# Kernel tuning notes

Hardware: AMD Instinct MI355X
Metric: run time of the kernel (lower is better)

Reference implementation:

```python
import jax, jax.numpy as jnp
import numpy as np

NUM_HEADS = 8
NEG_INF = -1e9  # stand-in for -inf in the causal mask (avoids nan under masked softmax)


def setup_inputs() -> dict:
    key = jax.random.key(0)
    ks = jax.random.split(key, 8)
    B, C, H, W = 2, 512, 64, 64
    E = 512
    s = 1.0 / np.sqrt(C)
    return {
        "query": jax.random.normal(ks[0], (B, C, H, W), jnp.float32),
        "key": jax.random.normal(ks[1], (B, C, H, W), jnp.float32),
        "Wq": jax.random.normal(ks[2], (E, C), jnp.float32) * s,
        "bq": jax.random.normal(ks[3], (E,), jnp.float32) * 0.01,
        "Wk": jax.random.normal(ks[4], (E, C), jnp.float32) * s,
        "bk": jax.random.normal(ks[5], (E,), jnp.float32) * 0.01,
        "Wv": jax.random.normal(ks[6], (E, C), jnp.float32) * s,
        "bv": jax.random.normal(ks[7], (E,), jnp.float32) * 0.01,
    }


def reference(query, key, Wq, bq, Wk, bk, Wv, bv):
    B, qdim, H, W = query.shape
    N = H * W
    E = Wq.shape[0]
    nh = NUM_HEADS
    hd = E // nh

    # (B, C, H, W) -> (B, N, C)
    q_tok = query.transpose(0, 2, 3, 1).reshape(B, N, qdim)
    k_tok = key.transpose(0, 2, 3, 1).reshape(B, N, key.shape[1])

    q = (q_tok @ Wq.T + bq).reshape(B, N, nh, hd)
    k = (k_tok @ Wk.T + bk).reshape(B, N, nh, hd)
    v = (k_tok @ Wv.T + bv).reshape(B, N, nh, hd)

    # scores: (B, heads, N, N)
    scores = jnp.einsum("bqhd,bkhd->bhqk", q, k) / jnp.sqrt(jnp.float32(hd))
    causal = jnp.tril(jnp.ones((N, N), dtype=bool))
    scores = jnp.where(causal, scores, NEG_INF)
    attn = jax.nn.softmax(scores, axis=-1)  # dropout p=0.0 -> identity

    x = jnp.einsum("bhqk,bkhd->bhqd", attn, v)  # (B, h, N, hd)
    # permute to (B, h, hd, N) then view as (B, E, H, W) — matches torch ordering
    out = x.transpose(0, 1, 3, 2).reshape(B, E, H, W)
    return out
```

## Files before the change

kernel.cpp:

```cpp
#include <hip/hip_runtime.h>


typedef __bf16 bf16;
typedef __attribute__((ext_vector_type(8))) __bf16 bf16x8;
typedef __attribute__((ext_vector_type(4))) float floatx4;

#define B_ 2
#define Cc 512
#define Nn 4096
#define Ee 512
#define NH 8
#define HD 64

#define QSCALE 0.1803368801111204f

#define WSEG 262144
#define WTOT 787968

__device__ __forceinline__ int probe_f32(const unsigned short* w, int tid) {
  bool bad = false;
#pragma unroll
  for (int i = 0; i < 16; ++i) {
    unsigned u = w[(tid & 63) * 16 + i];
    float v = __uint_as_float(u << 16);
    bad |= !(v > -1024.f && v < 1024.f);
  }
  return (__ballot(bad) != 0ull) ? 1 : 0;
}

__device__ __forceinline__ bf16x8 load8e(const void* base, size_t eidx, int f32) {
  if (!f32) return *(const bf16x8*)((const bf16*)base + eidx);
  const float* f = (const float*)base + eidx;
  float4 a = *(const float4*)f;
  float4 c = *(const float4*)(f + 4);
  union { bf16 h[8]; bf16x8 v; } u;
  u.h[0] = (bf16)a.x; u.h[1] = (bf16)a.y; u.h[2] = (bf16)a.z; u.h[3] = (bf16)a.w;
  u.h[4] = (bf16)c.x; u.h[5] = (bf16)c.y; u.h[6] = (bf16)c.z; u.h[7] = (bf16)c.w;
  return u.v;
}

__global__ __launch_bounds__(256) void prep(
    const void* __restrict__ X0, const void* __restrict__ X1,
    bf16* __restrict__ T0, bf16* __restrict__ T1,
    const float* __restrict__ Wq, const float* __restrict__ Wk,
    const float* __restrict__ Wv, const float* __restrict__ bq,
    const float* __restrict__ bk, const float* __restrict__ bv,
    bf16* __restrict__ Wb) {
  const int f32 = probe_f32((const unsigned short*)Wq, (int)threadIdx.x);
  if (blockIdx.z == 4) {
    if (!f32) return;
    int task = (int)blockIdx.y * 64 + (int)blockIdx.x;
    int idx = (task * 256 + (int)threadIdx.x) * 8;
    if (idx >= WTOT) return;
    const float* src;
    int off;
    if (idx < WSEG)            { src = Wq; off = idx; }
    else if (idx < 2 * WSEG)   { src = Wk; off = idx - WSEG; }
    else if (idx < 3 * WSEG)   { src = Wv; off = idx - 2 * WSEG; }
    else if (idx < 3 * WSEG + 512)  { src = bq; off = idx - 3 * WSEG; }
    else if (idx < 3 * WSEG + 1024) { src = bk; off = idx - 3 * WSEG - 512; }
    else                            { src = bv; off = idx - 3 * WSEG - 1024; }
    float4 a = *(const float4*)(src + off);
    float4 c = *(const float4*)(src + off + 4);
    union { bf16 h[8]; bf16x8 v; } u;
    u.h[0] = (bf16)a.x; u.h[1] = (bf16)a.y; u.h[2] = (bf16)a.z; u.h[3] = (bf16)a.w;
    u.h[4] = (bf16)c.x; u.h[5] = (bf16)c.y; u.h[6] = (bf16)c.z; u.h[7] = (bf16)c.w;
    *(bf16x8*)(Wb + idx) = u.v;
    return;
  }
  __shared__ __align__(16) bf16 T[64 * 64];
  const int z = blockIdx.z;
  const int bb = z & 1;
  const void* src = (z >> 1) ? X1 : X0;
  bf16* dst = (z >> 1) ? T1 : T0;
  const int n0 = blockIdx.x * 64, c0 = blockIdx.y * 64;
  const int t = threadIdx.x;
  const size_t sbase = ((size_t)bb * Cc + c0) * (size_t)Nn + n0;

#pragma unroll
  for (int it = 0; it < 2; ++it) {
    int task = t + it * 256;
    int crow = task >> 3, gr = task & 7;
    bf16x8 v = load8e(src, sbase + (size_t)crow * Nn + gr * 8, f32);
    int slot = gr ^ (crow & 7);
    *(bf16x8*)&T[crow * 64 + slot * 8] = v;
  }
  __syncthreads();
  const int nrow = t & 63, cp = t >> 6;
  bf16* db = dst + ((size_t)bb * Nn + n0 + nrow) * Cc + c0;
#pragma unroll
  for (int it = 0; it < 2; ++it) {
    int cg = cp * 2 + it;
    union { bf16 h[8]; bf16x8 v; } u;
#pragma unroll
    for (int j = 0; j < 8; ++j) {
      int c = cg * 8 + j;
      int slot = (nrow >> 3) ^ (c & 7);
      u.h[j] = T[c * 64 + slot * 8 + (nrow & 7)];
    }
    *(bf16x8*)(db + cg * 8) = u.v;
  }
}

__global__ __launch_bounds__(256) void gemm3(
    const bf16* __restrict__ Xtq, const bf16* __restrict__ Xtk,
    const void* __restrict__ Wq0, const bf16* __restrict__ Wqb,
    const void* __restrict__ Wk0, const bf16* __restrict__ Wkb,
    const void* __restrict__ Wv0, const bf16* __restrict__ Wvb,
    const void* __restrict__ bq0, const bf16* __restrict__ bqb,
    const void* __restrict__ bk0, const bf16* __restrict__ bkb,
    const void* __restrict__ bv0, const bf16* __restrict__ bvb,
    bf16* __restrict__ Qt, bf16* __restrict__ Kt, bf16* __restrict__ Vh,
    int zoff) {
  const int f32 = probe_f32((const unsigned short*)Wq0, (int)threadIdx.x);
  const int z = (int)blockIdx.z + zoff;
  const int op = z >> 1, b = z & 1;
  const bf16 *A, *Bt, *bias;
  bf16* Out;
  long sAb, sBb, sOb;
  int Nq, biasOnM, m0, n0;
  float scaleOut;
  if (op == 0) {
    A = Xtq; sAb = (long)Nn * Cc;
    Bt = f32 ? Wqb : (const bf16*)Wq0; sBb = 0;
    bias = f32 ? bqb : (const bf16*)bq0;
    Out = Qt; sOb = (long)Nn * Ee; Nq = Ee; biasOnM = 0; scaleOut = QSCALE;
    m0 = blockIdx.x * 128; n0 = blockIdx.y * 128;
  } else if (op == 1) {
    A = Xtk; sAb = (long)Nn * Cc;
    Bt = f32 ? Wkb : (const bf16*)Wk0; sBb = 0;
    bias = f32 ? bkb : (const bf16*)bk0;
    Out = Kt; sOb = (long)Nn * Ee; Nq = Ee; biasOnM = 0; scaleOut = 1.0f;
    m0 = blockIdx.x * 128; n0 = blockIdx.y * 128;
  } else {
    A = f32 ? Wvb : (const bf16*)Wv0; sAb = 0;
    Bt = Xtk; sBb = (long)Nn * Cc;
    bias = f32 ? bvb : (const bf16*)bv0;
    Out = Vh; sOb = (long)Ee * Nn; Nq = Nn; biasOnM = 1; scaleOut = 1.0f;
    m0 = blockIdx.y * 128;
    n0 = blockIdx.x * 128;
  }
  constexpr int K = 512;
  constexpr int SA = 40;
  __shared__ __align__(16) bf16 As[2][128 * SA];
  __shared__ __align__(16) bf16 Bs[2][128 * SA];
  const int tid = threadIdx.x;
  const int lane = tid & 63, wave = tid >> 6;
  const int quad = lane >> 4, lm = lane & 15;
  const bf16* Ab = A + (size_t)b * sAb;
  const bf16* Bb = Bt + (size_t)b * sBb;
  bf16* Ob = Out + (size_t)b * sOb;

  const int arow = tid >> 2, ag = tid & 3;

  floatx4 acc[2][8];
#pragma unroll
  for (int i = 0; i < 2; ++i)
#pragma unroll
    for (int j = 0; j < 8; ++j) acc[i][j] = (floatx4){0.f, 0.f, 0.f, 0.f};

  bf16x8 pa0[2], pa1[2], pb0[2], pb1[2];
#define LOADG(s, step)                                                      \
  do {                                                                      \
    const int k0_ = (step) * 32;                                            \
    pa0[s] = *(const bf16x8*)(Ab + (size_t)(m0 + arow) * K + k0_ + ag * 8); \
    pa1[s] = *(const bf16x8*)(Ab + (size_t)(m0 + 64 + arow) * K + k0_ + ag * 8); \
    pb0[s] = *(const bf16x8*)(Bb + (size_t)(n0 + arow) * K + k0_ + ag * 8); \
    pb1[s] = *(const bf16x8*)(Bb + (size_t)(n0 + 64 + arow) * K + k0_ + ag * 8); \
  } while (0)
#define STAGEG(s, c_)                                                       \
  do {                                                                      \
    *(bf16x8*)&As[c_][arow * SA + ag * 8] = pa0[s];                         \
    *(bf16x8*)&As[c_][(64 + arow) * SA + ag * 8] = pa1[s];                  \
    *(bf16x8*)&Bs[c_][arow * SA + ag * 8] = pb0[s];                         \
    *(bf16x8*)&Bs[c_][(64 + arow) * SA + ag * 8] = pb1[s];                  \
  } while (0)

  LOADG(0, 0);
  LOADG(1, 1);
  STAGEG(0, 0);
  __syncthreads();

  for (int kk = 0; kk < 16; kk += 2) {
#pragma unroll
    for (int u = 0; u < 2; ++u) {
      const int t = kk + u;
      if (t + 2 < 16) LOADG(u, t + 2);
      bf16x8 af[2];
#pragma unroll
      for (int mf = 0; mf < 2; ++mf) {
        int r = wave * 32 + mf * 16 + lm;
        af[mf] = *(const bf16x8*)&As[u][r * SA + quad * 8];
      }
      if (t + 1 < 16) STAGEG(u ^ 1, u ^ 1);
#pragma unroll
      for (int nf = 0; nf < 8; ++nf) {
        int r = nf * 16 + lm;
        bf16x8 bfr = *(const bf16x8*)&Bs[u][r * SA + quad * 8];
        acc[0][nf] = __builtin_amdgcn_mfma_f32_16x16x32_bf16(
            af[0], bfr, acc[0][nf], 0, 0, 0);
        acc[1][nf] = __builtin_amdgcn_mfma_f32_16x16x32_bf16(
            af[1], bfr, acc[1][nf], 0, 0, 0);
      }
      __syncthreads();
    }
  }
#undef LOADG
#undef STAGEG

#pragma unroll
  for (int mf = 0; mf < 2; ++mf) {
#pragma unroll
    for (int nf = 0; nf < 8; ++nf) {
      int col = n0 + nf * 16 + lm;
      float bn = biasOnM ? 0.f : (float)bias[col];
#pragma unroll
      for (int r = 0; r < 4; ++r) {
        int rowg = m0 + wave * 32 + mf * 16 + quad * 4 + r;
        float bv = biasOnM ? (float)bias[rowg] : bn;
        Ob[(size_t)rowg * Nq + col] = (bf16)((acc[mf][nf][r] + bv) * scaleOut);
      }
    }
  }
}

__device__ __forceinline__ float fast_exp2(float x) {
  return __builtin_amdgcn_exp2f(x);
}
__device__ __forceinline__ unsigned pack_bf16_2(float a, float b) {
  unsigned ua = __float_as_uint(a) + 0x8000u;
  unsigned ub = __float_as_uint(b) + 0x8000u;
  return (ua >> 16) | (ub & 0xFFFF0000u);
}

__global__ __launch_bounds__(256, 4) void attn(
    const bf16* __restrict__ Qt, const bf16* __restrict__ Kt,
    const bf16* __restrict__ Ve, void* __restrict__ Out,
    const unsigned short* __restrict__ wdet) {
  const int tid = threadIdx.x, lane = tid & 63, w = tid >> 6;
  const int f32 = probe_f32(wdet, tid);
  constexpr int SK = 72;
  __shared__ __align__(16) bf16 Ks[2][64 * SK];
  __shared__ __align__(16) bf16 Vs[2][64 * SK];
  const int quad = lane >> 4, lm = lane & 15;

  const int L = (int)blockIdx.x + 64 * (int)blockIdx.y + 512 * (int)blockIdx.z;
  const int xcd = L & 7, slot0 = L >> 3;
  const int half = slot0 >> 6, sp = slot0 & 63;
  const int p = half ? 63 - sp : sp;
  const int hp = xcd * 2 + half;
  const int b = hp >> 3, h = hp & 7;

  const int Q0 = p * 64;
  const int qbase = Q0 + w * 16;
  const int last = p;

  bf16x8 qf[2];
  {
    const bf16* qp =
        Qt + ((size_t)b * Nn + qbase + lm) * Ee + h * HD + quad * 8;
    qf[0] = *(const bf16x8*)qp;
    qf[1] = *(const bf16x8*)(qp + 32);
  }
  floatx4 accO[4];
#pragma unroll
  for (int df = 0; df < 4; ++df) accO[df] = (floatx4){0.f, 0.f, 0.f, 0.f};
  float lsum = 0.f;

  const int r0 = tid >> 3, g = tid & 7;
  const int sslot = ((g + r0) & 7) * 8;
  const bf16* kp0 = Kt + ((size_t)b * Nn + r0) * Ee + h * HD + g * 8;
  const bf16* kp1 = kp0 + (size_t)32 * Ee;
  const bf16* vp0 = Ve + ((size_t)b * Ee + h * HD + r0) * Nn + g * 8;
  const bf16* vp1 = vp0 + (size_t)32 * Nn;

  const int rbase = ((lm >> 2) << 3) | (lm & 3);

  bf16x8 ka[2], kb[2], va[2], vb[2];
#define LOADT(s)                                                   \
  do {                                                             \
    ka[s] = *(const bf16x8*)kp0; kb[s] = *(const bf16x8*)kp1;      \
    va[s] = *(const bf16x8*)vp0; vb[s] = *(const bf16x8*)vp1;      \
    kp0 += (size_t)64 * Ee; kp1 += (size_t)64 * Ee;                \
    vp0 += 64; vp1 += 64;                                          \
  } while (0)
#define STAGET(s, buf)                                             \
  do {                                                             \
    *(bf16x8*)&Ks[buf][r0 * SK + sslot] = ka[s];                   \
    *(bf16x8*)&Ks[buf][(r0 + 32) * SK + sslot] = kb[s];            \
    *(bf16x8*)&Vs[buf][r0 * SK + sslot] = va[s];                   \
    *(bf16x8*)&Vs[buf][(r0 + 32) * SK + sslot] = vb[s];            \
  } while (0)

  LOADT(0);
  if (last >= 1) LOADT(1);
  STAGET(0, 0);
  __syncthreads();

#pragma unroll 1
  for (int kt = 0; kt <= last; kt += 2) {
#pragma unroll
    for (int u = 0; u < 2; ++u) {
      const int t = kt + u;
      if (u == 1 && t > last) break;
      const int k0 = t * 64;
      if (t + 2 <= last) LOADT(u);
      const bool skip = k0 > qbase + 15;

      bf16x8 pb[2];
      if (!skip) {
        floatx4 accS[4];
#pragma unroll
        for (int f = 0; f < 4; ++f) accS[f] = (floatx4){0.f, 0.f, 0.f, 0.f};
        __builtin_amdgcn_s_setprio(1);
#pragma unroll
        for (int ks = 0; ks < 2; ++ks)
#pragma unroll
          for (int f = 0; f < 4; ++f) {
            const int R = rbase + ((f & 1) << 2) + ((f >> 1) << 5);
            const int sl = (ks * 4 + quad + R) & 7;
            bf16x8 ak = *(const bf16x8*)&Ks[u][R * SK + sl * 8];
            accS[f] = __builtin_amdgcn_mfma_f32_16x16x32_bf16(
                ak, qf[ks], accS[f], 0, 0, 0);
          }
        __builtin_amdgcn_s_setprio(0);
        const bool maskt = (k0 + 63 > qbase);
        if (!maskt) {
          float la = 0.f, lb = 0.f;
#pragma unroll
          for (int g2 = 0; g2 < 2; ++g2) {
            union { unsigned pk[4]; bf16x8 v; } uu;
#pragma unroll
            for (int jp = 0; jp < 4; ++jp) {
              const int fidx = g2 * 2 + (jp >> 1);
              const int re = (jp & 1) * 2;
              float p0 = fast_exp2(accS[fidx][re]);
              float p1 = fast_exp2(accS[fidx][re + 1]);
              la += p0; lb += p1;
              uu.pk[jp] = pack_bf16_2(p0, p1);
            }
            pb[g2] = uu.v;
          }
          lsum += la + lb;
        } else {
          const int qg = qbase + lm;
          float la = 0.f, lb = 0.f;
#pragma unroll
          for (int g2 = 0; g2 < 2; ++g2) {
            union { unsigned pk[4]; bf16x8 v; } uu;
#pragma unroll
            for (int jp = 0; jp < 4; ++jp) {
              const int fidx = g2 * 2 + (jp >> 1);
              const int re = (jp & 1) * 2;
              const int key0 = k0 + g2 * 32 + quad * 8 + jp * 2;
              float p0 = fast_exp2(accS[fidx][re]);
              float p1 = fast_exp2(accS[fidx][re + 1]);
              if (key0 > qg) p0 = 0.f;
              if (key0 + 1 > qg) p1 = 0.f;
              la += p0; lb += p1;
              uu.pk[jp] = pack_bf16_2(p0, p1);
            }
            pb[g2] = uu.v;
          }
          lsum += la + lb;
        }
      }
      if (t + 1 <= last) STAGET(u ^ 1, u ^ 1);
      if (!skip) {
        __builtin_amdgcn_s_setprio(1);
#pragma unroll
        for (int g2 = 0; g2 < 2; ++g2)
#pragma unroll
          for (int df = 0; df < 4; ++df) {
            const int Rv = df * 16 + lm;
            const int sl = (g2 * 4 + quad + Rv) & 7;
            bf16x8 av = *(const bf16x8*)&Vs[u][Rv * SK + sl * 8];
            accO[df] = __builtin_amdgcn_mfma_f32_16x16x32_bf16(
                av, pb[g2], accO[df], 0, 0, 0);
          }
        __builtin_amdgcn_s_setprio(0);
      }
      __syncthreads();
    }
  }
#undef LOADT
#undef STAGET

  lsum += __shfl_xor(lsum, 16);
  lsum += __shfl_xor(lsum, 32);

  const float inv = 1.0f / lsum;
  const int qg = qbase + lm;
#pragma unroll
  for (int df = 0; df < 4; ++df) {
#pragma unroll
    for (int r = 0; r < 4; ++r) {
      int d = h * HD + df * 16 + quad * 4 + r;
      size_t off = ((size_t)b * Ee + d) * Nn + qg;
      if (!f32) ((bf16*)Out)[off] = (bf16)(accO[df][r] * inv);
      else      ((float*)Out)[off] = accO[df][r] * inv;
    }
  }
}

extern "C" void kernel_launch(void* const* d_in, const int* in_sizes, int n_in,
                              void* d_out, int out_size, void* d_ws,
                              size_t ws_size, hipStream_t stream) {
  const void* q  = d_in[0];
  const void* k  = d_in[1];
  const void* Wq = d_in[2];
  const void* bq = d_in[3];
  const void* Wk = d_in[4];
  const void* bk = d_in[5];
  const void* Wv = d_in[6];
  const void* bv = d_in[7];

  const size_t SZ = (size_t)B_ * Nn * Cc;
  bf16* Xtq  = (bf16*)((char*)d_ws + 1024);
  bf16* Qt   = Xtq + SZ;
  bf16* Kt   = Qt + SZ;
  bf16* Xtk  = (bf16*)d_out;
  bf16* Wb   = (bf16*)((char*)d_out + 8 * 1024 * 1024);
  bf16* Wqb = Wb,            *Wkb = Wb + WSEG,    *Wvb = Wb + 2 * WSEG;
  bf16* bqb = Wb + 3 * WSEG, *bkb = bqb + 512,    *bvb = bqb + 1024;

  const size_t need = 1024 + 4 * SZ * sizeof(bf16);
  const bool sep = ws_size >= need;
  bf16* Vh = sep ? (Kt + SZ) : Xtq;

  prep<<<dim3(64, 8, 5), 256, 0, stream>>>(
      q, k, Xtq, Xtk,
      (const float*)Wq, (const float*)Wk, (const float*)Wv,
      (const float*)bq, (const float*)bk, (const float*)bv, Wb);
  if (sep) {
    gemm3<<<dim3(32, 4, 6), 256, 0, stream>>>(
        Xtq, Xtk, Wq, Wqb, Wk, Wkb, Wv, Wvb,
        bq, bqb, bk, bkb, bv, bvb, Qt, Kt, Vh, 0);
  } else {
    gemm3<<<dim3(32, 4, 4), 256, 0, stream>>>(
        Xtq, Xtk, Wq, Wqb, Wk, Wkb, Wv, Wvb,
        bq, bqb, bk, bkb, bv, bvb, Qt, Kt, Vh, 0);
    gemm3<<<dim3(32, 4, 2), 256, 0, stream>>>(
        Xtq, Xtk, Wq, Wqb, Wk, Wkb, Wv, Wvb,
        bq, bqb, bk, bkb, bv, bvb, Qt, Kt, Vh, 4);
  }
  attn<<<dim3(64, NH, B_), 256, 0, stream>>>(
      Qt, Kt, Vh, d_out, (const unsigned short*)Wq);
}
```

Baseline: 175.9 us.

## Load projection GEMM tiles straight to LDS with swizzled layout

The projection GEMM now uses global_load_lds to copy A and B tiles directly from global memory into shared memory, rather than staging them through registers and storing them afterwards. The padded row stride is dropped so each lane's destination is contiguous. A rotation swizzle on the global chunk index, undone at read time, avoids LDS bank conflicts. This frees registers and removes the separate LDS store step, but correctness now depends on the asynchronous LDS writes finishing before the barrier. The attention kernel, which likely dominates total time, is unchanged.

```diff
diff --git a/kernel.cpp b/kernel.cpp
--- a/kernel.cpp
+++ b/kernel.cpp
@@ -26,6 +26,12 @@
     bad |= !(v > -1024.f && v < 1024.f);
   }
   return (__ballot(bad) != 0ull) ? 1 : 0;
+}
+
+__device__ __forceinline__ void gll16(const bf16* g, bf16* l) {
+  __builtin_amdgcn_global_load_lds(
+      (const __attribute__((address_space(1))) void*)g,
+      (__attribute__((address_space(3))) void*)l, 16, 0, 0);
 }
 
 __device__ __forceinline__ bf16x8 load8e(const void* base, size_t eidx, int f32) {
@@ -141,7 +147,7 @@
     n0 = blockIdx.x * 128;
   }
   constexpr int K = 512;
-  constexpr int SA = 40;
+  constexpr int SA = 32;
   __shared__ __align__(16) bf16 As[2][128 * SA];
   __shared__ __align__(16) bf16 Bs[2][128 * SA];
   const int tid = threadIdx.x;
@@ -152,61 +158,52 @@
   bf16* Ob = Out + (size_t)b * sOb;
 
   const int arow = tid >> 2, ag = tid & 3;
-
+  const int gsw = (ag + arow) & 3;
   floatx4 acc[2][8];
 #pragma unroll
   for (int i = 0; i < 2; ++i)
 #pragma unroll
     for (int j = 0; j < 8; ++j) acc[i][j] = (floatx4){0.f, 0.f, 0.f, 0.f};
 
-  bf16x8 pa0[2], pa1[2], pb0[2], pb1[2];
-#define LOADG(s, step)                                                      \
-  do {                                                                      \
-    const int k0_ = (step) * 32;                                            \
-    pa0[s] = *(const bf16x8*)(Ab + (size_t)(m0 + arow) * K + k0_ + ag * 8); \
-    pa1[s] = *(const bf16x8*)(Ab + (size_t)(m0 + 64 + arow) * K + k0_ + ag * 8); \
-    pb0[s] = *(const bf16x8*)(Bb + (size_t)(n0 + arow) * K + k0_ + ag * 8); \
-    pb1[s] = *(const bf16x8*)(Bb + (size_t)(n0 + 64 + arow) * K + k0_ + ag * 8); \
+#define ISSUE(step, c_)                                                      \
+  do {                                                                       \
+    const int k0_ = (step) * 32 + gsw * 8;                                   \
+    gll16(Ab + (size_t)(m0 + arow) * K + k0_,                                \
+          &As[c_][arow * SA + ag * 8]);                                      \
+    gll16(Ab + (size_t)(m0 + 64 + arow) * K + k0_,                           \
+          &As[c_][(64 + arow) * SA + ag * 8]);                               \
+    gll16(Bb + (size_t)(n0 + arow) * K + k0_,                                \
+          &Bs[c_][arow * SA + ag * 8]);                                      \
+    gll16(Bb + (size_t)(n0 + 64 + arow) * K + k0_,                           \
+          &Bs[c_][(64 + arow) * SA + ag * 8]);                               \
   } while (0)
-#define STAGEG(s, c_)                                                       \
-  do {                                                                      \
-    *(bf16x8*)&As[c_][arow * SA + ag * 8] = pa0[s];                         \
-    *(bf16x8*)&As[c_][(64 + arow) * SA + ag * 8] = pa1[s];                  \
-    *(bf16x8*)&Bs[c_][arow * SA + ag * 8] = pb0[s];                         \
-    *(bf16x8*)&Bs[c_][(64 + arow) * SA + ag * 8] = pb1[s];                  \
-  } while (0)
-
-  LOADG(0, 0);
-  LOADG(1, 1);
-  STAGEG(0, 0);
+
+  ISSUE(0, 0);
   __syncthreads();
 
-  for (int kk = 0; kk < 16; kk += 2) {
-#pragma unroll
-    for (int u = 0; u < 2; ++u) {
-      const int t = kk + u;
-      if (t + 2 < 16) LOADG(u, t + 2);
-      bf16x8 af[2];
-#pragma unroll
-      for (int mf = 0; mf < 2; ++mf) {
-        int r = wave * 32 + mf * 16 + lm;
-        af[mf] = *(const bf16x8*)&As[u][r * SA + quad * 8];
-      }
-      if (t + 1 < 16) STAGEG(u ^ 1, u ^ 1);
-#pragma unroll
-      for (int nf = 0; nf < 8; ++nf) {
-        int r = nf * 16 + lm;
-        bf16x8 bfr = *(const bf16x8*)&Bs[u][r * SA + quad * 8];
-        acc[0][nf] = __builtin_amdgcn_mfma_f32_16x16x32_bf16(
-            af[0], bfr, acc[0][nf], 0, 0, 0);
-        acc[1][nf] = __builtin_amdgcn_mfma_f32_16x16x32_bf16(
-            af[1], bfr, acc[1][nf], 0, 0, 0);
-      }
-      __syncthreads();
-    }
-  }
-#undef LOADG
-#undef STAGEG
+  for (int kk = 0; kk < 16; ++kk) {
+    const int c = kk & 1;
+    if (kk + 1 < 16) ISSUE(kk + 1, c ^ 1);
+    bf16x8 af[2];
+#pragma unroll
+    for (int mf = 0; mf < 2; ++mf) {
+      int r = wave * 32 + mf * 16 + lm;
+      int sa = (quad - r) & 3;
+      af[mf] = *(const bf16x8*)&As[c][r * SA + sa * 8];
+    }
+#pragma unroll
+    for (int nf = 0; nf < 8; ++nf) {
+      int rn = nf * 16 + lm;
+      int sb = (quad - rn) & 3;
+      bf16x8 bfr = *(const bf16x8*)&Bs[c][rn * SA + sb * 8];
+      acc[0][nf] = __builtin_amdgcn_mfma_f32_16x16x32_bf16(
+          af[0], bfr, acc[0][nf], 0, 0, 0);
+      acc[1][nf] = __builtin_amdgcn_mfma_f32_16x16x32_bf16(
+          af[1], bfr, acc[1][nf], 0, 0, 0);
+    }
+    __syncthreads();
+  }
+#undef ISSUE
 
 #pragma unroll
   for (int mf = 0; mf < 2; ++mf) {
```

Result: no change. 175.9 us, median of 2 (-0.0%).
